# Kernel tuning notes

Hardware: AMD Instinct MI355X
Metric: run time of the kernel (lower is better)

Reference implementation:

```python
import jax, jax.numpy as jnp
import numpy as np

D_MODEL = 1024
H = 16
D_K = D_MODEL // H  # 64
B, S = 2, 2048


def setup_inputs() -> dict:
    key = jax.random.key(0)
    ks = jax.random.split(key, 8)
    scale = 1.0 / np.sqrt(D_MODEL)
    return {
        "q": jax.random.normal(ks[0], (B, S, D_MODEL), dtype=jnp.float32),
        "k": jax.random.normal(ks[1], (B, S, D_MODEL), dtype=jnp.float32),
        "v": jax.random.normal(ks[2], (B, S, D_MODEL), dtype=jnp.float32),
        "W_q": jax.random.normal(ks[3], (H, D_MODEL, D_K), dtype=jnp.float32) * scale,
        "W_k": jax.random.normal(ks[4], (H, D_MODEL, D_K), dtype=jnp.float32) * scale,
        "W_v": jax.random.normal(ks[5], (H, D_MODEL, D_K), dtype=jnp.float32) * scale,
        "W_o": jax.random.normal(ks[6], (D_MODEL, H * D_K), dtype=jnp.float32) * scale,
        "b_o": jnp.zeros((D_MODEL,), dtype=jnp.float32),
    }


def reference(q, k, v, W_q, W_k, W_v, W_o, b_o):
    b, s, _ = q.shape
    h, _, d_k = W_q.shape
    inv_sqrt_dk = jnp.asarray(1.0 / np.sqrt(d_k), q.dtype)
    # per-head projections: [b, h, s, d_k]
    qh = jnp.einsum("bsd,hdk->bhsk", q, W_q)
    kh = jnp.einsum("bsd,hdk->bhsk", k, W_k)
    vh = jnp.einsum("bsd,hdk->bhsk", v, W_v)
    # scaled dot product attention
    scores = jnp.einsum("bhqk,bhsk->bhqs", qh, kh) * inv_sqrt_dk  # [b,h,S,S]
    attn = jax.nn.softmax(scores, axis=-1)
    ctx = jnp.einsum("bhqs,bhsk->bhqk", attn, vh)  # [b,h,S,d_k]
    # chunk over heads + concat along feature dim -> [b, S, h*d_k], head-major
    ctx = ctx.transpose(0, 2, 1, 3).reshape(b, s, h * d_k)
    # final linear
    return ctx @ W_o.T + b_o
```

## Files before the change

kernel.cpp:

```cpp
#include <hip/hip_runtime.h>
#include <cstdint>
#include <cstddef>


typedef unsigned short bf16_t;
typedef __attribute__((ext_vector_type(8))) short short8;
typedef __attribute__((ext_vector_type(4))) float f32x4;

__device__ __forceinline__ uint32_t fbits(float f) {
  union { float f; uint32_t u; } v; v.f = f; return v.u;
}
__device__ __forceinline__ bf16_t f2bf(float f) {
  uint32_t u = fbits(f);
  return (bf16_t)((u + 0x7FFFu + ((u >> 16) & 1u)) >> 16);
}
__device__ __forceinline__ uint32_t packbf2(float lo, float hi) {
  uint32_t a = fbits(hi) + 0x8000u;
  uint32_t b = fbits(lo) + 0x8000u;
  return __builtin_amdgcn_perm(a, b, 0x07060302u);
}

__global__ void prep_kernel(const float* __restrict__ q, const float* __restrict__ k,
                            const float* __restrict__ v, const float* __restrict__ Wo,
                            const float* __restrict__ Wq, const float* __restrict__ Wk,
                            const float* __restrict__ Wv,
                            bf16_t* __restrict__ qo, bf16_t* __restrict__ ko,
                            bf16_t* __restrict__ vo, bf16_t* __restrict__ Woo,
                            bf16_t* __restrict__ Wtq, bf16_t* __restrict__ Wtk,
                            bf16_t* __restrict__ Wtv) {
  int blk = blockIdx.x;
  int tid = threadIdx.x;
  if (blk < 13312) {
    const float* src; bf16_t* dst; int i;
    if (blk < 4096)       { src = q;  dst = qo;  i = blk * 256 + tid; }
    else if (blk < 8192)  { src = k;  dst = ko;  i = (blk - 4096) * 256 + tid; }
    else if (blk < 12288) { src = v;  dst = vo;  i = (blk - 8192) * 256 + tid; }
    else                  { src = Wo; dst = Woo; i = (blk - 12288) * 256 + tid; }
    f32x4 val = ((const f32x4*)src)[i];
    ushort4 o;
    o.x = f2bf(val.x); o.y = f2bf(val.y); o.z = f2bf(val.z); o.w = f2bf(val.w);
    ((ushort4*)dst)[i] = o;
  } else {
    int blk2 = blk - 13312;
    int z = blk2 >> 9, t = blk2 & 511;
    const float* W = z == 0 ? Wq : z == 1 ? Wk : Wv;
    bf16_t* Wt = z == 0 ? Wtq : z == 1 ? Wtk : Wtv;
    int h = t >> 5, d0 = (t & 31) * 32;
    __shared__ float tile[32][65];
    const float* src = W + ((size_t)h << 16) + (size_t)d0 * 64;
    int d = tid >> 3;
#pragma unroll
    for (int j = 0; j < 2; j++) {
      int dk = (tid & 7) * 8 + j * 4;
      *(f32x4*)&tile[d][dk] = *(const f32x4*)(src + d * 64 + dk);
    }
    __syncthreads();
    int dk2 = tid >> 2, c = tid & 3;
    union { ushort s[8]; int4 v; } o;
#pragma unroll
    for (int j = 0; j < 8; j++) o.s[j] = f2bf(tile[c * 8 + j][dk2]);
    *(int4*)(Wt + (size_t)(h * 64 + dk2) * 1024 + d0 + c * 8) = o.v;
  }
}

__global__ __launch_bounds__(256) void gemm_proj_kernel(
    const bf16_t* __restrict__ A0, const bf16_t* __restrict__ A1, const bf16_t* __restrict__ A2,
    const bf16_t* __restrict__ B0, const bf16_t* __restrict__ B1, const bf16_t* __restrict__ B2,
    bf16_t* __restrict__ O0, bf16_t* __restrict__ O1, bf16_t* __restrict__ O2,
    float s0)
{
  const int z = blockIdx.z;
  const bf16_t* A  = z == 0 ? A0 : z == 1 ? A1 : A2;
  const bf16_t* Bt = z == 0 ? B0 : z == 1 ? B1 : B2;
  bf16_t* Cout     = z == 0 ? O0 : z == 1 ? O1 : O2;
  const float scale = z == 0 ? s0 : 1.0f;
  const int K = 1024;

  __shared__ alignas(16) bf16_t smem[18432];

  const int tid = threadIdx.x;
  const int lane = tid & 63, wave = tid >> 6;
  const int wm = wave >> 1, wn = wave & 1;
  const int quad = lane >> 4, l15 = lane & 15;
  const int m0 = blockIdx.y * 128, n0 = blockIdx.x * 128;

  f32x4 acc[4][4];
#pragma unroll
  for (int i = 0; i < 4; i++)
#pragma unroll
    for (int j = 0; j < 4; j++) acc[i][j] = (f32x4)0.0f;

  const int c0 = wave * 128 + lane;
  const int c1 = c0 + 64;
  const bf16_t* pa0 = A  + (size_t)(m0 + (c0 >> 2)) * K + (c0 & 3) * 8;
  const bf16_t* pa1 = A  + (size_t)(m0 + (c1 >> 2)) * K + (c1 & 3) * 8;
  const bf16_t* pb0 = Bt + (size_t)(n0 + (c0 >> 2)) * K + (c0 & 3) * 8;
  const bf16_t* pb1 = Bt + (size_t)(n0 + (c1 >> 2)) * K + (c1 & 3) * 8;
  const int s0a = c0 * 8, s1a = c1 * 8;

  int4 ra0 = *(const int4*)pa0;
  int4 ra1 = *(const int4*)pa1;
  int4 rb0 = *(const int4*)pb0;
  int4 rb1 = *(const int4*)pb1;
  *(int4*)(smem + s0a) = ra0;
  *(int4*)(smem + s1a) = ra1;
  *(int4*)(smem + 4096 + s0a) = rb0;
  *(int4*)(smem + 4096 + s1a) = rb1;
  __syncthreads();

  for (int it = 0; it < 32; ++it) {
    const int co = (it & 1) * 8192;
    if (it < 31) {
      const int ko = (it + 1) * 32;
      ra0 = *(const int4*)(pa0 + ko);
      ra1 = *(const int4*)(pa1 + ko);
      rb0 = *(const int4*)(pb0 + ko);
      rb1 = *(const int4*)(pb1 + ko);
    }

    short8 af[4], bfr[4];
#pragma unroll
    for (int mi = 0; mi < 4; mi++)
      af[mi] = *(const short8*)(smem + co + (wm * 64 + mi * 16 + l15) * 32 + quad * 8);
#pragma unroll
    for (int ni = 0; ni < 4; ni++)
      bfr[ni] = *(const short8*)(smem + co + 4096 + (wn * 64 + ni * 16 + l15) * 32 + quad * 8);
#pragma unroll
    for (int mi = 0; mi < 4; mi++)
#pragma unroll
      for (int ni = 0; ni < 4; ni++)
        acc[mi][ni] = __builtin_amdgcn_mfma_f32_16x16x32_bf16(af[mi], bfr[ni], acc[mi][ni], 0, 0, 0);

    if (it < 31) {
      const int no = ((it + 1) & 1) * 8192;
      *(int4*)(smem + no + s0a) = ra0;
      *(int4*)(smem + no + s1a) = ra1;
      *(int4*)(smem + no + 4096 + s0a) = rb0;
      *(int4*)(smem + no + 4096 + s1a) = rb1;
    }
    __syncthreads();
  }

  const int s0r = m0 & 2047, bb = m0 >> 11, hp = n0 >> 6;
  if (z < 2) {
    bf16_t* slot = smem + wn * 9216;
#pragma unroll
    for (int ni = 0; ni < 4; ni++)
#pragma unroll
      for (int mi = 0; mi < 4; mi++)
#pragma unroll
        for (int r = 0; r < 4; r++)
          slot[(wm * 64 + mi * 16 + quad * 4 + r) * 72 + ni * 16 + l15] =
              f2bf(acc[mi][ni][r] * scale);
    __syncthreads();
#pragma unroll
    for (int rd = 0; rd < 8; ++rd) {
      int idx = rd * 256 + tid;
      int si = idx >> 10, mm = (idx >> 3) & 127, c8 = idx & 7;
      int4 val = *(const int4*)(smem + si * 9216 + mm * 72 + c8 * 8);
      *(int4*)(Cout + ((size_t)((bb * 16 + hp + si) * 2048 + s0r + mm)) * 64 + c8 * 8) = val;
    }
  } else {
    bf16_t* slot = smem + wn * 8704;
#pragma unroll
    for (int ni = 0; ni < 4; ni++)
#pragma unroll
      for (int mi = 0; mi < 4; mi++) {
        uint2 pk = make_uint2(packbf2(acc[mi][ni][0], acc[mi][ni][1]),
                              packbf2(acc[mi][ni][2], acc[mi][ni][3]));
        *(uint2*)(slot + (ni * 16 + l15) * 136 + wm * 64 + mi * 16 + quad * 4) = pk;
      }
    __syncthreads();
#pragma unroll
    for (int rd = 0; rd < 8; ++rd) {
      int idx = rd * 256 + tid;
      int si = idx >> 10, c = (idx >> 4) & 63, ck = idx & 15;
      int4 val = *(const int4*)(smem + si * 8704 + c * 136 + ck * 8);
      *(int4*)(Cout + (size_t)(bb * 16 + hp + si) * 131072 + (size_t)c * 2048 + s0r + ck * 8) = val;
    }
  }
}

__global__ __launch_bounds__(256) void gemm_out_kernel(
    const bf16_t* __restrict__ A, const bf16_t* __restrict__ Bt,
    float* __restrict__ C, const float* __restrict__ bias)
{
  const int K = 1024, N = 1024;
  __shared__ alignas(16) bf16_t smem[12288];
  const int tid = threadIdx.x;
  const int lane = tid & 63, wave = tid >> 6;
  const int quad = lane >> 4, l15 = lane & 15;
  const int m0 = blockIdx.y * 128, n0 = blockIdx.x * 64;

  f32x4 acc[2][4];
#pragma unroll
  for (int i = 0; i < 2; i++)
#pragma unroll
    for (int j = 0; j < 4; j++) acc[i][j] = (f32x4)0.0f;

  const int c0 = wave * 128 + lane, c1 = c0 + 64;
  const int cb = wave * 64 + lane;
  const bf16_t* pa0 = A  + (size_t)(m0 + (c0 >> 2)) * K + (c0 & 3) * 8;
  const bf16_t* pa1 = A  + (size_t)(m0 + (c1 >> 2)) * K + (c1 & 3) * 8;
  const bf16_t* pb  = Bt + (size_t)(n0 + (cb >> 2)) * K + (cb & 3) * 8;
  const int s0a = c0 * 8, s1a = c1 * 8, sba = cb * 8;

  int4 ra0 = *(const int4*)pa0;
  int4 ra1 = *(const int4*)pa1;
  int4 rb  = *(const int4*)pb;
  *(int4*)(smem + s0a) = ra0;
  *(int4*)(smem + s1a) = ra1;
  *(int4*)(smem + 4096 + sba) = rb;
  __syncthreads();

  for (int it = 0; it < 32; ++it) {
    const int co = (it & 1) * 6144;
    if (it < 31) {
      const int ko = (it + 1) * 32;
      ra0 = *(const int4*)(pa0 + ko);
      ra1 = *(const int4*)(pa1 + ko);
      rb  = *(const int4*)(pb + ko);
    }

    short8 af[2], bfr[4];
#pragma unroll
    for (int mi = 0; mi < 2; mi++)
      af[mi] = *(const short8*)(smem + co + (wave * 32 + mi * 16 + l15) * 32 + quad * 8);
#pragma unroll
    for (int ni = 0; ni < 4; ni++)
      bfr[ni] = *(const short8*)(smem + co + 4096 + (ni * 16 + l15) * 32 + quad * 8);
#pragma unroll
    for (int mi = 0; mi < 2; mi++)
#pragma unroll
      for (int ni = 0; ni < 4; ni++)
        acc[mi][ni] = __builtin_amdgcn_mfma_f32_16x16x32_bf16(af[mi], bfr[ni], acc[mi][ni], 0, 0, 0);

    if (it < 31) {
      const int no = ((it + 1) & 1) * 6144;
      *(int4*)(smem + no + s0a) = ra0;
      *(int4*)(smem + no + s1a) = ra1;
      *(int4*)(smem + no + 4096 + sba) = rb;
    }
    __syncthreads();
  }

#pragma unroll
  for (int ni = 0; ni < 4; ni++) {
    int col = n0 + ni * 16 + l15;
    float bv = bias[col];
#pragma unroll
    for (int mi = 0; mi < 2; mi++) {
      int row = m0 + wave * 32 + mi * 16 + quad * 4;
#pragma unroll
      for (int r = 0; r < 4; r++)
        C[(size_t)(row + r) * N + col] = acc[mi][ni][r] + bv;
    }
  }
}

__global__ __launch_bounds__(512) void flash_kernel(
    const bf16_t* __restrict__ qh, const bf16_t* __restrict__ kh,
    const bf16_t* __restrict__ vT, bf16_t* __restrict__ ctx)
{
  __shared__ alignas(16) bf16_t KtF[2][4096];
  __shared__ alignas(16) bf16_t VtF[2][4096];
  __shared__ alignas(16) bf16_t PtF[8 * 1024];
  const int tid = threadIdx.x, lane = tid & 63, wave = tid >> 6;
  const int quad = lane >> 4, l15 = lane & 15;
  const int q0 = blockIdx.x * 128;
  const int h = blockIdx.y, b = blockIdx.z;
  const size_t headoff = (size_t)(b * 16 + h) * 2048 * 64;
  const bf16_t* Q = qh + headoff;
  const bf16_t* K = kh + headoff;
  const bf16_t* V = vT + headoff;

  const int qrow = q0 + wave * 16 + l15;
  short8 qf[2];
#pragma unroll
  for (int ks = 0; ks < 2; ks++)
    qf[ks] = *(const short8*)(Q + (size_t)qrow * 64 + ks * 32 + quad * 8);

  f32x4 O[4];
#pragma unroll
  for (int mi = 0; mi < 4; mi++) O[mi] = (f32x4)0.0f;
  f32x4 lacc = (f32x4)0.0f;

  const bf16_t* Kp = K + (size_t)((wave >> 1) * 16 + l15) * 64 + (wave & 1) * 32 + quad * 8;
  const bf16_t* Vp = V + (size_t)((wave >> 1) * 16 + l15) * 2048 + (wave & 1) * 32 + quad * 8;
  const int soff = wave * 512 + lane * 8;

  const int pwbase = wave * 2048 + ((quad >> 1) * 16 + l15) * 16 + 8 * (quad & 1);

  int4 kreg = *(const int4*)Kp;
  int4 vreg = *(const int4*)Vp;
  *(int4*)(&KtF[0][soff]) = kreg;
  *(int4*)(&VtF[0][soff]) = vreg;
  __syncthreads();

  for (int it = 0; it < 32; ++it) {
    const int cur = it & 1, nxt = cur ^ 1;
    if (it < 31) {
      kreg = *(const int4*)(Kp + (size_t)(it + 1) * 4096);
      vreg = *(const int4*)(Vp + (it + 1) * 64);
    }

    f32x4 S[4];
#pragma unroll
    for (int mi = 0; mi < 4; mi++) S[mi] = (f32x4)0.0f;
#pragma unroll
    for (int ks = 0; ks < 2; ks++) {
#pragma unroll
      for (int mi = 0; mi < 4; mi++) {
        short8 kf = *(const short8*)(&KtF[cur][(mi * 2 + ks) * 512 + lane * 8]);
        S[mi] = __builtin_amdgcn_mfma_f32_16x16x32_bf16(kf, qf[ks], S[mi], 0, 0, 0);
      }
    }

#pragma unroll
    for (int mi = 0; mi < 4; mi++)
#pragma unroll
      for (int r = 0; r < 4; r++)
        S[mi][r] = __builtin_amdgcn_exp2f(S[mi][r]);
    lacc += (S[0] + S[1]) + (S[2] + S[3]);

#pragma unroll
    for (int mi = 0; mi < 4; mi++) {
      uint2 pk = make_uint2(packbf2(S[mi][0], S[mi][1]), packbf2(S[mi][2], S[mi][3]));
      *(uint2*)((char*)PtF + pwbase + (mi >> 1) * 1024 + (mi & 1) * 512) = pk;
    }

#pragma unroll
    for (int ks = 0; ks < 2; ks++) {
      short8 pfrag = *(const short8*)(&PtF[wave * 1024 + (ks * 64 + lane) * 8]);
#pragma unroll
      for (int mi = 0; mi < 4; mi++) {
        short8 vf = *(const short8*)(&VtF[cur][(mi * 2 + ks) * 512 + lane * 8]);
        O[mi] = __builtin_amdgcn_mfma_f32_16x16x32_bf16(vf, pfrag, O[mi], 0, 0, 0);
      }
    }

    if (it < 31) {
      *(int4*)(&KtF[nxt][soff]) = kreg;
      *(int4*)(&VtF[nxt][soff]) = vreg;
    }
    __syncthreads();
  }

  float l = (lacc[0] + lacc[1]) + (lacc[2] + lacc[3]);
  l += __shfl_xor(l, 16, 64);
  l += __shfl_xor(l, 32, 64);
  float inv = 1.0f / l;
  bf16_t* crow = ctx + ((size_t)(b * 2048 + qrow)) * 1024 + h * 64;
#pragma unroll
  for (int mi = 0; mi < 4; mi++) {
    uint2 pk = make_uint2(packbf2(O[mi][0] * inv, O[mi][1] * inv),
                          packbf2(O[mi][2] * inv, O[mi][3] * inv));
    *(uint2*)(crow + mi * 16 + quad * 4) = pk;
  }
}

extern "C" void kernel_launch(void* const* d_in, const int* in_sizes, int n_in,
                              void* d_out, int out_size, void* d_ws, size_t ws_size,
                              hipStream_t stream)
{
  const float* q  = (const float*)d_in[0];
  const float* k  = (const float*)d_in[1];
  const float* v  = (const float*)d_in[2];
  const float* Wq = (const float*)d_in[3];
  const float* Wk = (const float*)d_in[4];
  const float* Wv = (const float*)d_in[5];
  const float* Wo = (const float*)d_in[6];
  const float* bo = (const float*)d_in[7];
  float* out = (float*)d_out;

  const size_t NX = (size_t)4096 * 1024;
  const size_t NW = (size_t)1024 * 1024;

  char* p = (char*)d_ws;
  bf16_t* qbf = (bf16_t*)p; p += NX * 2;
  bf16_t* kbf = (bf16_t*)p; p += NX * 2;
  bf16_t* vbf = (bf16_t*)p; p += NX * 2;
  bf16_t* Wtq = (bf16_t*)p; p += NW * 2;
  bf16_t* Wtk = (bf16_t*)p; p += NW * 2;
  bf16_t* Wtv = (bf16_t*)p; p += NW * 2;
  bf16_t* Wob = (bf16_t*)p; p += NW * 2;
  bf16_t* qhb = (bf16_t*)p; p += NX * 2;
  bf16_t* khb = (bf16_t*)p; p += NX * 2;
  bf16_t* vTb = (bf16_t*)p; p += NX * 2;
  bf16_t* ctxb = (bf16_t*)p; p += NX * 2;

  prep_kernel<<<14848, 256, 0, stream>>>(q, k, v, Wo, Wq, Wk, Wv,
                                         qbf, kbf, vbf, Wob, Wtq, Wtk, Wtv);

  const float qscale = 0.125f * 1.44269504088896340736f;
  gemm_proj_kernel<<<dim3(8, 32, 3), 256, 0, stream>>>(qbf, kbf, vbf, Wtq, Wtk, Wtv,
                                                       qhb, khb, vTb, qscale);

  flash_kernel<<<dim3(16, 16, 2), 512, 0, stream>>>(qhb, khb, vTb, ctxb);

  gemm_out_kernel<<<dim3(16, 32), 256, 0, stream>>>(ctxb, Wob, out, bo);

  (void)in_sizes; (void)n_in; (void)out_size; (void)ws_size;
}
```

Measured before the change: 217.6 us.

## Process two query tiles per wave in flash kernel to reuse K/V fragments

Each wave now handles 32 query rows (two 16-row groups) instead of 16, so each K and V fragment loaded from shared memory feeds two MFMAs. The block covers 256 queries and the grid is halved, which doubles the reuse of each K/V tile staged into LDS. The cost is more registers per thread for the doubled S/O accumulators, a larger P buffer in shared memory, and fewer blocks (256) on the device, which may hurt occupancy.

After: 218.3 us. About the same (+0.3%).

```diff
diff --git a/kernel.cpp b/kernel.cpp
--- a/kernel.cpp
+++ b/kernel.cpp
@@ -264,32 +264,36 @@
 {
   __shared__ alignas(16) bf16_t KtF[2][4096];
   __shared__ alignas(16) bf16_t VtF[2][4096];
-  __shared__ alignas(16) bf16_t PtF[8 * 1024];
+  __shared__ alignas(16) bf16_t PtF[16384];
   const int tid = threadIdx.x, lane = tid & 63, wave = tid >> 6;
   const int quad = lane >> 4, l15 = lane & 15;
-  const int q0 = blockIdx.x * 128;
+  const int q0 = blockIdx.x * 256;
   const int h = blockIdx.y, b = blockIdx.z;
   const size_t headoff = (size_t)(b * 16 + h) * 2048 * 64;
   const bf16_t* Q = qh + headoff;
   const bf16_t* K = kh + headoff;
   const bf16_t* V = vT + headoff;
 
-  const int qrow = q0 + wave * 16 + l15;
-  short8 qf[2];
-#pragma unroll
-  for (int ks = 0; ks < 2; ks++)
-    qf[ks] = *(const short8*)(Q + (size_t)qrow * 64 + ks * 32 + quad * 8);
-
-  f32x4 O[4];
-#pragma unroll
-  for (int mi = 0; mi < 4; mi++) O[mi] = (f32x4)0.0f;
-  f32x4 lacc = (f32x4)0.0f;
+  short8 qf[2][2];
+#pragma unroll
+  for (int g = 0; g < 2; g++)
+#pragma unroll
+    for (int ks = 0; ks < 2; ks++)
+      qf[g][ks] = *(const short8*)(Q + (size_t)(q0 + wave * 32 + g * 16 + l15) * 64
+                                   + ks * 32 + quad * 8);
+
+  f32x4 O[2][4];
+#pragma unroll
+  for (int g = 0; g < 2; g++)
+#pragma unroll
+    for (int mi = 0; mi < 4; mi++) O[g][mi] = (f32x4)0.0f;
+  f32x4 lacc[2] = {(f32x4)0.0f, (f32x4)0.0f};
 
   const bf16_t* Kp = K + (size_t)((wave >> 1) * 16 + l15) * 64 + (wave & 1) * 32 + quad * 8;
   const bf16_t* Vp = V + (size_t)((wave >> 1) * 16 + l15) * 2048 + (wave & 1) * 32 + quad * 8;
   const int soff = wave * 512 + lane * 8;
 
-  const int pwbase = wave * 2048 + ((quad >> 1) * 16 + l15) * 16 + 8 * (quad & 1);
+  const int pwb = wave * 4096 + ((quad >> 1) * 16 + l15) * 16 + 8 * (quad & 1);
 
   int4 kreg = *(const int4*)Kp;
   int4 vreg = *(const int4*)Vp;
@@ -304,38 +308,49 @@
       vreg = *(const int4*)(Vp + (it + 1) * 64);
     }
 
-    f32x4 S[4];
-#pragma unroll
-    for (int mi = 0; mi < 4; mi++) S[mi] = (f32x4)0.0f;
+    f32x4 S[2][4];
+#pragma unroll
+    for (int g = 0; g < 2; g++)
+#pragma unroll
+      for (int mi = 0; mi < 4; mi++) S[g][mi] = (f32x4)0.0f;
 #pragma unroll
     for (int ks = 0; ks < 2; ks++) {
 #pragma unroll
       for (int mi = 0; mi < 4; mi++) {
         short8 kf = *(const short8*)(&KtF[cur][(mi * 2 + ks) * 512 + lane * 8]);
-        S[mi] = __builtin_amdgcn_mfma_f32_16x16x32_bf16(kf, qf[ks], S[mi], 0, 0, 0);
+        S[0][mi] = __builtin_amdgcn_mfma_f32_16x16x32_bf16(kf, qf[0][ks], S[0][mi], 0, 0, 0);
+        S[1][mi] = __builtin_amdgcn_mfma_f32_16x16x32_bf16(kf, qf[1][ks], S[1][mi], 0, 0, 0);
       }
     }
 
 #pragma unroll
-    for (int mi = 0; mi < 4; mi++)
-#pragma unroll
-      for (int r = 0; r < 4; r++)
-        S[mi][r] = __builtin_amdgcn_exp2f(S[mi][r]);
-    lacc += (S[0] + S[1]) + (S[2] + S[3]);
-
-#pragma unroll
-    for (int mi = 0; mi < 4; mi++) {
-      uint2 pk = make_uint2(packbf2(S[mi][0], S[mi][1]), packbf2(S[mi][2], S[mi][3]));
-      *(uint2*)((char*)PtF + pwbase + (mi >> 1) * 1024 + (mi & 1) * 512) = pk;
-    }
+    for (int g = 0; g < 2; g++) {
+#pragma unroll
+      for (int mi = 0; mi < 4; mi++)
+#pragma unroll
+        for (int r = 0; r < 4; r++)
+          S[g][mi][r] = __builtin_amdgcn_exp2f(S[g][mi][r]);
+      lacc[g] += (S[g][0] + S[g][1]) + (S[g][2] + S[g][3]);
+    }
+
+#pragma unroll
+    for (int g = 0; g < 2; g++)
+#pragma unroll
+      for (int mi = 0; mi < 4; mi++) {
+        uint2 pk = make_uint2(packbf2(S[g][mi][0], S[g][mi][1]),
+                              packbf2(S[g][mi][2], S[g][mi][3]));
+        *(uint2*)((char*)PtF + pwb + g * 2048 + (mi >> 1) * 1024 + (mi & 1) * 512) = pk;
+      }
 
 #pragma unroll
     for (int ks = 0; ks < 2; ks++) {
-      short8 pfrag = *(const short8*)(&PtF[wave * 1024 + (ks * 64 + lane) * 8]);
+      short8 pf0 = *(const short8*)(&PtF[wave * 2048 + (ks * 64 + lane) * 8]);
+      short8 pf1 = *(const short8*)(&PtF[wave * 2048 + 1024 + (ks * 64 + lane) * 8]);
 #pragma unroll
       for (int mi = 0; mi < 4; mi++) {
         short8 vf = *(const short8*)(&VtF[cur][(mi * 2 + ks) * 512 + lane * 8]);
-        O[mi] = __builtin_amdgcn_mfma_f32_16x16x32_bf16(vf, pfrag, O[mi], 0, 0, 0);
+        O[0][mi] = __builtin_amdgcn_mfma_f32_16x16x32_bf16(vf, pf0, O[0][mi], 0, 0, 0);
+        O[1][mi] = __builtin_amdgcn_mfma_f32_16x16x32_bf16(vf, pf1, O[1][mi], 0, 0, 0);
       }
     }
 
@@ -346,16 +361,20 @@
     __syncthreads();
   }
 
-  float l = (lacc[0] + lacc[1]) + (lacc[2] + lacc[3]);
-  l += __shfl_xor(l, 16, 64);
-  l += __shfl_xor(l, 32, 64);
-  float inv = 1.0f / l;
-  bf16_t* crow = ctx + ((size_t)(b * 2048 + qrow)) * 1024 + h * 64;
-#pragma unroll
-  for (int mi = 0; mi < 4; mi++) {
-    uint2 pk = make_uint2(packbf2(O[mi][0] * inv, O[mi][1] * inv),
-                          packbf2(O[mi][2] * inv, O[mi][3] * inv));
-    *(uint2*)(crow + mi * 16 + quad * 4) = pk;
+#pragma unroll
+  for (int g = 0; g < 2; g++) {
+    float l = (lacc[g][0] + lacc[g][1]) + (lacc[g][2] + lacc[g][3]);
+    l += __shfl_xor(l, 16, 64);
+    l += __shfl_xor(l, 32, 64);
+    float inv = 1.0f / l;
+    int qrow = q0 + wave * 32 + g * 16 + l15;
+    bf16_t* crow = ctx + ((size_t)(b * 2048 + qrow)) * 1024 + h * 64;
+#pragma unroll
+    for (int mi = 0; mi < 4; mi++) {
+      uint2 pk = make_uint2(packbf2(O[g][mi][0] * inv, O[g][mi][1] * inv),
+                            packbf2(O[g][mi][2] * inv, O[g][mi][3] * inv));
+      *(uint2*)(crow + mi * 16 + quad * 4) = pk;
+    }
   }
 }
 
@@ -396,7 +415,7 @@
   gemm_proj_kernel<<<dim3(8, 32, 3), 256, 0, stream>>>(qbf, kbf, vbf, Wtq, Wtk, Wtv,
                                                        qhb, khb, vTb, qscale);
 
-  flash_kernel<<<dim3(16, 16, 2), 512, 0, stream>>>(qhb, khb, vTb, ctxb);
+  flash_kernel<<<dim3(8, 16, 2), 512, 0, stream>>>(qhb, khb, vTb, ctxb);
 
   gemm_out_kernel<<<dim3(16, 32), 256, 0, stream>>>(ctxb, Wob, out, bo);
 
```
